# Optimization experiments

Measured on AMD Instinct MI355X. Metric: run time of the kernel, lower is better.

## Reference

```python
import jax, jax.numpy as jnp
import numpy as np

N = 50000      # nodes
E = 800000     # edges (before self loops)
D_IN = 128
HID = 64
HEADS = 8
D_OUT = 10


def setup_inputs() -> dict:
    key = jax.random.key(0)
    ks = jax.random.split(key, 16)
    sc = 0.05
    x = jax.random.normal(ks[0], (N, D_IN), dtype=jnp.float32)
    edge_index = jax.random.randint(ks[1], (2, E), 0, N, dtype=jnp.int64)
    return {
        "x": x,
        "edge_index": edge_index,
        "W1": jax.random.normal(ks[2], (HEADS * HID, D_IN), dtype=jnp.float32) * sc,
        "a1_src": jax.random.normal(ks[3], (HEADS, HID), dtype=jnp.float32) * sc,
        "a1_dst": jax.random.normal(ks[4], (HEADS, HID), dtype=jnp.float32) * sc,
        "b1": jnp.zeros((HEADS * HID,), jnp.float32),
        "W2": jax.random.normal(ks[5], (HID, HEADS * HID), dtype=jnp.float32) * sc,
        "a2_src": jax.random.normal(ks[6], (1, HID), dtype=jnp.float32) * sc,
        "a2_dst": jax.random.normal(ks[7], (1, HID), dtype=jnp.float32) * sc,
        "b2": jnp.zeros((HID,), jnp.float32),
        "W3": jax.random.normal(ks[8], (HID, HID), dtype=jnp.float32) * sc,
        "a3_src": jax.random.normal(ks[9], (1, HID), dtype=jnp.float32) * sc,
        "a3_dst": jax.random.normal(ks[10], (1, HID), dtype=jnp.float32) * sc,
        "b3": jnp.zeros((HID,), jnp.float32),
        "Wc": jax.random.normal(ks[11], (D_OUT, HID), dtype=jnp.float32) * sc,
        "bc": jnp.zeros((D_OUT,), jnp.float32),
    }


def gat_conv(x, src, dst, W, a_src, a_dst, b, concat):
    """PyG GATConv (eval mode, add_self_loops already applied to src/dst)."""
    heads, out_ch = a_src.shape
    n = x.shape[0]
    h = (x @ W.T).reshape(n, heads, out_ch)          # [N, H, C]
    a_s = jnp.einsum('nhc,hc->nh', h, a_src)          # [N, H]
    a_d = jnp.einsum('nhc,hc->nh', h, a_dst)          # [N, H]
    e = jax.nn.leaky_relu(a_s[src] + a_d[dst], 0.2)   # [Etot, H]
    # segment softmax over incoming edges of each destination node
    m = jax.ops.segment_max(e, dst, num_segments=n)
    ex = jnp.exp(e - m[dst])
    s = jax.ops.segment_sum(ex, dst, num_segments=n)
    alpha = ex / (s[dst] + 1e-16)                     # [Etot, H]
    out = jax.ops.segment_sum(h[src] * alpha[:, :, None], dst, num_segments=n)
    if concat:
        out = out.reshape(n, heads * out_ch)
    else:
        out = out.mean(axis=1)
    return out + b


def reference(x, edge_index, W1, a1_src, a1_dst, b1, W2, a2_src, a2_dst, b2,
              W3, a3_src, a3_dst, b3, Wc, bc):
    loops = jnp.arange(N, dtype=edge_index.dtype)
    src = jnp.concatenate([edge_index[0], loops])
    dst = jnp.concatenate([edge_index[1], loops])
    h = jax.nn.elu(gat_conv(x, src, dst, W1, a1_src, a1_dst, b1, True))
    h = jax.nn.elu(gat_conv(h, src, dst, W2, a2_src, a2_dst, b2, False))
    h = jax.nn.elu(gat_conv(h, src, dst, W3, a3_src, a3_dst, b3, False))
    return h @ Wc.T + bc
```

## Files before the change

### kernel.cpp

```cpp
#include <hip/hip_runtime.h>
#include <math.h>

#define N_NODES 50000
#define N_EDGES 800000
#define ETOT    (N_EDGES + N_NODES)

typedef short bf16x8 __attribute__((ext_vector_type(8)));
typedef float f32x4  __attribute__((ext_vector_type(4)));
typedef float f32x2  __attribute__((ext_vector_type(2)));

__device__ __forceinline__ float b2f(unsigned int u16) {
    return __uint_as_float(u16 << 16);
}
__device__ __forceinline__ unsigned short f2b(float f) {
    unsigned int u = __float_as_uint(f);
    u += 0x7fffu + ((u >> 16) & 1u);
    return (unsigned short)(u >> 16);
}

__global__ __launch_bounds__(256) void k_prep(const float* __restrict__ x,
                                              const float* __restrict__ w1,
                                              const float* __restrict__ w2,
                                              const float* __restrict__ w3,
                                              unsigned short* __restrict__ xb,
                                              unsigned short* __restrict__ o1,
                                              unsigned short* __restrict__ o2,
                                              unsigned short* __restrict__ o3,
                                              int* __restrict__ deg,
                                              int* __restrict__ flag) {
    int i = blockIdx.x * 256 + threadIdx.x;
    if (i < N_NODES) deg[i] = 0;
    if (i == 0) *flag = 0;
    if (i < 512 * 128 / 4) {
        float4 v = ((const float4*)w1)[i];
        ushort2* o = (ushort2*)(o1 + i * 4);
        o[0] = make_ushort2(f2b(v.x), f2b(v.y));
        o[1] = make_ushort2(f2b(v.z), f2b(v.w));
    }
    if (i < 64 * 512 / 4) {
        float4 v = ((const float4*)w2)[i];
        ushort2* o = (ushort2*)(o2 + i * 4);
        o[0] = make_ushort2(f2b(v.x), f2b(v.y));
        o[1] = make_ushort2(f2b(v.z), f2b(v.w));
    }
    if (i < 64 * 64 / 4) {
        float4 v = ((const float4*)w3)[i];
        ushort2* o = (ushort2*)(o3 + i * 4);
        o[0] = make_ushort2(f2b(v.x), f2b(v.y));
        o[1] = make_ushort2(f2b(v.z), f2b(v.w));
    }
    if (i < N_NODES * 128 / 8) {
        const float4* xp = (const float4*)x + (size_t)i * 2;
        float4 v0 = xp[0], v1 = xp[1];
        unsigned int u0 = (unsigned int)f2b(v0.x) | ((unsigned int)f2b(v0.y) << 16);
        unsigned int u1 = (unsigned int)f2b(v0.z) | ((unsigned int)f2b(v0.w) << 16);
        unsigned int u2 = (unsigned int)f2b(v1.x) | ((unsigned int)f2b(v1.y) << 16);
        unsigned int u3 = (unsigned int)f2b(v1.z) | ((unsigned int)f2b(v1.w) << 16);
        *(uint4*)(xb + (size_t)i * 8) = make_uint4(u0, u1, u2, u3);
    }
}

__global__ void k_detect(const int* __restrict__ idx, int* __restrict__ flag) {
    int i = blockIdx.x * blockDim.x + threadIdx.x;
    int v = idx[2 * i + 1];
    unsigned long long any = __ballot(v != 0);
    if ((threadIdx.x & 63) == 0 && any) atomicOr(flag, 1);
}

__device__ __forceinline__ int edge_src(const int* idx, int e, int is32) {
    return is32 ? idx[e] : idx[2 * e];
}
__device__ __forceinline__ int edge_dst(const int* idx, int e, int is32) {
    return is32 ? idx[N_EDGES + e] : idx[2 * (N_EDGES + e)];
}

__global__ void k_degree(const int* __restrict__ idx, const int* __restrict__ flag,
                         int* __restrict__ deg) {
    int e = blockIdx.x * blockDim.x + threadIdx.x;
    if (e >= ETOT) return;
    int is32 = *flag;
    int d = (e < N_EDGES) ? edge_dst(idx, e, is32) : (e - N_EDGES);
    atomicAdd(&deg[d], 1);
}

__global__ __launch_bounds__(256) void k_scan1(const int* __restrict__ deg,
                                               int* __restrict__ rowptr,
                                               int* __restrict__ bsum) {
    __shared__ int sd[256];
    int t = threadIdx.x;
    int i = blockIdx.x * 256 + t;
    int v = (i < N_NODES) ? deg[i] : 0;
    sd[t] = v;
    __syncthreads();
#pragma unroll
    for (int off = 1; off < 256; off <<= 1) {
        int a = (t >= off) ? sd[t - off] : 0;
        __syncthreads();
        sd[t] += a;
        __syncthreads();
    }
    if (i < N_NODES) rowptr[i] = sd[t] - v;
    if (t == 255) bsum[blockIdx.x] = sd[255];
}

__global__ __launch_bounds__(256) void k_scan2(int* __restrict__ bsum,
                                               int* __restrict__ boff,
                                               int* __restrict__ rowptr,
                                               int nb) {
    __shared__ int sd[256];
    int t = threadIdx.x;
    int v = (t < nb) ? bsum[t] : 0;
    sd[t] = v;
    __syncthreads();
#pragma unroll
    for (int off = 1; off < 256; off <<= 1) {
        int a = (t >= off) ? sd[t - off] : 0;
        __syncthreads();
        sd[t] += a;
        __syncthreads();
    }
    boff[t] = sd[t] - v;
    if (t == 255) rowptr[N_NODES] = sd[255];
}

__global__ __launch_bounds__(256) void k_scan3(int* __restrict__ rowptr,
                                               const int* __restrict__ boff,
                                               int* __restrict__ cursor) {
    int i = blockIdx.x * 256 + threadIdx.x;
    if (i >= N_NODES) return;
    int r = rowptr[i] + boff[blockIdx.x];
    rowptr[i] = r;
    cursor[i] = r;
}

__global__ void k_scatter(const int* __restrict__ idx, const int* __restrict__ flag,
                          int* __restrict__ cursor, int* __restrict__ col) {
    int e = blockIdx.x * blockDim.x + threadIdx.x;
    if (e >= ETOT) return;
    int is32 = *flag;
    int s, d;
    if (e < N_EDGES) { s = edge_src(idx, e, is32); d = edge_dst(idx, e, is32); }
    else             { s = d = e - N_EDGES; }
    int pos = atomicAdd(&cursor[d], 1);
    col[pos] = s;
}

template<int AFP32>
__global__ __launch_bounds__(256) void k_gemm(const float* __restrict__ Af,
                                              const unsigned short* __restrict__ Ab,
                                              const unsigned short* __restrict__ W,
                                              unsigned short* __restrict__ C,
                                              const float* __restrict__ a_src,
                                              const float* __restrict__ a_dst,
                                              float* __restrict__ asb,
                                              float* __restrict__ adb,
                                              int M, int K, int Nout, int Hstr) {
    __shared__ unsigned short As[64 * 40];
    __shared__ unsigned short Bs[64 * 40];
    __shared__ float red_s[4][64];
    __shared__ float red_d[4][64];
    int t = threadIdx.x;
    int w = t >> 6, l = t & 63;
    int quad = l >> 4, lm = l & 15;
    int m0 = blockIdx.y * 64, n0 = blockIdx.x * 64;
    int hd = blockIdx.x;
    int lr = t >> 2;
    int lc = (t & 3) * 8;

    f32x4 acc[4];
#pragma unroll
    for (int r = 0; r < 4; ++r) acc[r] = (f32x4){0.f, 0.f, 0.f, 0.f};

    for (int k0 = 0; k0 < K; k0 += 32) {
        int m = m0 + lr;
        if (AFP32) {
            float4 a0 = {0.f,0.f,0.f,0.f}, a1 = {0.f,0.f,0.f,0.f};
            if (m < M) {
                const float4* ap = (const float4*)(Af + (size_t)m * K + k0 + lc);
                a0 = ap[0]; a1 = ap[1];
            }
            unsigned int u0 = (unsigned int)f2b(a0.x) | ((unsigned int)f2b(a0.y) << 16);
            unsigned int u1 = (unsigned int)f2b(a0.z) | ((unsigned int)f2b(a0.w) << 16);
            unsigned int u2 = (unsigned int)f2b(a1.x) | ((unsigned int)f2b(a1.y) << 16);
            unsigned int u3 = (unsigned int)f2b(a1.z) | ((unsigned int)f2b(a1.w) << 16);
            *(uint4*)&As[lr * 40 + lc] = make_uint4(u0, u1, u2, u3);
        } else {
            uint4 av = make_uint4(0, 0, 0, 0);
            if (m < M) av = *(const uint4*)(Ab + (size_t)m * K + k0 + lc);
            *(uint4*)&As[lr * 40 + lc] = av;
        }
        uint4 bv = *(const uint4*)(W + (size_t)(n0 + lr) * K + k0 + lc);
        *(uint4*)&Bs[lr * 40 + lc] = bv;
        __syncthreads();

        bf16x8 bfrag = *(const bf16x8*)&Bs[(w * 16 + lm) * 40 + quad * 8];
#pragma unroll
        for (int r = 0; r < 4; ++r) {
            bf16x8 afrag = *(const bf16x8*)&As[(r * 16 + lm) * 40 + quad * 8];
            acc[r] = __builtin_amdgcn_mfma_f32_16x16x32_bf16(afrag, bfrag, acc[r], 0, 0, 0);
        }
        __syncthreads();
    }

#pragma unroll
    for (int r = 0; r < 4; ++r)
#pragma unroll
        for (int g = 0; g < 4; ++g) {
            int m = m0 + r * 16 + quad * 4 + g;
            if (m < M) C[(size_t)m * Nout + n0 + w * 16 + lm] = f2b(acc[r][g]);
        }

    float as = a_src[hd * 64 + w * 16 + lm];
    float ad = a_dst[hd * 64 + w * 16 + lm];
#pragma unroll
    for (int r = 0; r < 4; ++r) {
#pragma unroll
        for (int g = 0; g < 4; ++g) {
            float vs = acc[r][g] * as;
            float vd = acc[r][g] * ad;
#pragma unroll
            for (int off = 1; off < 16; off <<= 1) {
                vs += __shfl_xor(vs, off);
                vd += __shfl_xor(vd, off);
            }
            if (lm == 0) {
                red_s[w][r * 16 + quad * 4 + g] = vs;
                red_d[w][r * 16 + quad * 4 + g] = vd;
            }
        }
    }
    __syncthreads();
    if (t < 64) {
        float vs = red_s[0][t] + red_s[1][t] + red_s[2][t] + red_s[3][t];
        float vd = red_d[0][t] + red_d[1][t] + red_d[2][t] + red_d[3][t];
        int m = m0 + t;
        if (m < M) {
            asb[(size_t)m * Hstr + hd] = vs;
            adb[(size_t)m * Hstr + hd] = vd;
        }
    }
}

__device__ __forceinline__ void agg8_acc(float t, float adn, uint4 hv,
                                         float& ssum, f32x2* o2) {
    float e = t + adn;
    e = fmaxf(e, 0.2f * e);
    float ex = __expf(e);
    ssum += ex;
    f32x2 ex2 = {ex, ex};
    f32x2 f;
    f.x = __uint_as_float(hv.x << 16); f.y = __uint_as_float(hv.x & 0xffff0000u);
    asm("v_pk_fma_f32 %0, %1, %2, %0" : "+v"(o2[0]) : "v"(f), "v"(ex2));
    f.x = __uint_as_float(hv.y << 16); f.y = __uint_as_float(hv.y & 0xffff0000u);
    asm("v_pk_fma_f32 %0, %1, %2, %0" : "+v"(o2[1]) : "v"(f), "v"(ex2));
    f.x = __uint_as_float(hv.z << 16); f.y = __uint_as_float(hv.z & 0xffff0000u);
    asm("v_pk_fma_f32 %0, %1, %2, %0" : "+v"(o2[2]) : "v"(f), "v"(ex2));
    f.x = __uint_as_float(hv.w << 16); f.y = __uint_as_float(hv.w & 0xffff0000u);
    asm("v_pk_fma_f32 %0, %1, %2, %0" : "+v"(o2[3]) : "v"(f), "v"(ex2));
}

__global__ __launch_bounds__(256) void k_agg8(const unsigned short* __restrict__ h,
                                              const float* __restrict__ asrc,
                                              const float* __restrict__ adst,
                                              const int* __restrict__ rowptr,
                                              const int* __restrict__ col,
                                              const float* __restrict__ bias,
                                              unsigned short* __restrict__ out) {
    int n = blockIdx.x * 4 + (threadIdx.x >> 6);
    if (n >= N_NODES) return;
    int l = threadIdx.x & 63;
    int j = l >> 3;
    int lbase = l << 3;
    int start = rowptr[n], end = rowptr[n + 1];
    float adn = adst[(n << 3) + j];

    float ssum = 0.f;
    f32x2 o2[4];
#pragma unroll
    for (int i = 0; i < 4; ++i) o2[i] = (f32x2){0.f, 0.f};

    int k = start;
    int kA = (start + 3) & ~3;
    if (kA > end) kA = end;
    for (; k < kA; ++k) {
        int s = col[k];
        float t = asrc[((unsigned)s << 3) + (unsigned)j];
        uint4 hv = *(const uint4*)(h + ((unsigned)s << 9) + (unsigned)lbase);
        agg8_acc(t, adn, hv, ssum, o2);
    }
    int kEnd4 = kA + ((end - kA) & ~3);
    if (k < kEnd4) {
        int4 cN = *(const int4*)(col + k);
        for (; k < kEnd4; k += 4) {
            int4 c = cN;
            if (k + 8 <= kEnd4) cN = *(const int4*)(col + k + 4);
            float t0 = asrc[((unsigned)c.x << 3) + (unsigned)j];
            float t1 = asrc[((unsigned)c.y << 3) + (unsigned)j];
            float t2 = asrc[((unsigned)c.z << 3) + (unsigned)j];
            float t3 = asrc[((unsigned)c.w << 3) + (unsigned)j];
            uint4 hv0 = *(const uint4*)(h + ((unsigned)c.x << 9) + (unsigned)lbase);
            uint4 hv1 = *(const uint4*)(h + ((unsigned)c.y << 9) + (unsigned)lbase);
            uint4 hv2 = *(const uint4*)(h + ((unsigned)c.z << 9) + (unsigned)lbase);
            uint4 hv3 = *(const uint4*)(h + ((unsigned)c.w << 9) + (unsigned)lbase);
            agg8_acc(t0, adn, hv0, ssum, o2);
            agg8_acc(t1, adn, hv1, ssum, o2);
            agg8_acc(t2, adn, hv2, ssum, o2);
            agg8_acc(t3, adn, hv3, ssum, o2);
        }
    }
    for (; k < end; ++k) {
        int s = col[k];
        float t = asrc[((unsigned)s << 3) + (unsigned)j];
        uint4 hv = *(const uint4*)(h + ((unsigned)s << 9) + (unsigned)lbase);
        agg8_acc(t, adn, hv, ssum, o2);
    }

    float inv = 1.f / (ssum + 1e-16f);
    unsigned int p[4];
#pragma unroll
    for (int i = 0; i < 4; ++i) {
        float v0 = o2[i].x * inv + bias[lbase + 2 * i];
        float v1 = o2[i].y * inv + bias[lbase + 2 * i + 1];
        v0 = (v0 > 0.f) ? v0 : expm1f(v0);
        v1 = (v1 > 0.f) ? v1 : expm1f(v1);
        p[i] = (unsigned int)f2b(v0) | ((unsigned int)f2b(v1) << 16);
    }
    *(uint4*)(out + (size_t)n * 512 + lbase) = make_uint4(p[0], p[1], p[2], p[3]);
}

__global__ __launch_bounds__(256) void k_agg1(const unsigned short* __restrict__ h,
                                              const float* __restrict__ asrc,
                                              const float* __restrict__ adst,
                                              const int* __restrict__ rowptr,
                                              const int* __restrict__ col,
                                              const float* __restrict__ bias,
                                              unsigned short* __restrict__ out) {
    int n = blockIdx.x * 4 + (threadIdx.x >> 6);
    if (n >= N_NODES) return;
    int l = threadIdx.x & 63;
    int start = rowptr[n], end = rowptr[n + 1];
    float adn = adst[n];

    float ssum = 0.f, o = 0.f;
    int k = start;
    int kA = (start + 3) & ~3;
    if (kA > end) kA = end;
    for (; k < kA; ++k) {
        int s = col[k];
        float t = asrc[s];
        float hf = b2f(h[((unsigned)s << 6) + (unsigned)l]);
        float e = t + adn; e = fmaxf(e, 0.2f * e);
        float ex = __expf(e);
        ssum += ex; o += ex * hf;
    }
    int kEnd4 = kA + ((end - kA) & ~3);
    if (k < kEnd4) {
        int4 cN = *(const int4*)(col + k);
        for (; k < kEnd4; k += 4) {
            int4 c = cN;
            if (k + 8 <= kEnd4) cN = *(const int4*)(col + k + 4);
            float t0 = asrc[c.x], t1 = asrc[c.y], t2 = asrc[c.z], t3 = asrc[c.w];
            unsigned short q0 = h[((unsigned)c.x << 6) + (unsigned)l];
            unsigned short q1 = h[((unsigned)c.y << 6) + (unsigned)l];
            unsigned short q2 = h[((unsigned)c.z << 6) + (unsigned)l];
            unsigned short q3 = h[((unsigned)c.w << 6) + (unsigned)l];
            float e0 = t0 + adn; e0 = fmaxf(e0, 0.2f * e0);
            float ex0 = __expf(e0); ssum += ex0; o += ex0 * b2f(q0);
            float e1 = t1 + adn; e1 = fmaxf(e1, 0.2f * e1);
            float ex1 = __expf(e1); ssum += ex1; o += ex1 * b2f(q1);
            float e2 = t2 + adn; e2 = fmaxf(e2, 0.2f * e2);
            float ex2 = __expf(e2); ssum += ex2; o += ex2 * b2f(q2);
            float e3 = t3 + adn; e3 = fmaxf(e3, 0.2f * e3);
            float ex3 = __expf(e3); ssum += ex3; o += ex3 * b2f(q3);
        }
    }
    for (; k < end; ++k) {
        int s = col[k];
        float t = asrc[s];
        float hf = b2f(h[((unsigned)s << 6) + (unsigned)l]);
        float e = t + adn; e = fmaxf(e, 0.2f * e);
        float ex = __expf(e);
        ssum += ex; o += ex * hf;
    }
    float v = o / (ssum + 1e-16f) + bias[l];
    v = (v > 0.f) ? v : expm1f(v);
    out[(size_t)n * 64 + l] = f2b(v);
}

__global__ __launch_bounds__(256) void k_classifier(const unsigned short* __restrict__ h,
                                                    const float* __restrict__ Wc,
                                                    const float* __restrict__ bc,
                                                    float* __restrict__ out) {
    __shared__ float sW[640];
    for (int i = threadIdx.x; i < 640; i += blockDim.x) sW[i] = Wc[i];
    __syncthreads();
    int idx = blockIdx.x * blockDim.x + threadIdx.x;
    if (idx >= N_NODES * 10) return;
    int n = idx / 10, d = idx - n * 10;
    const unsigned short* hr = h + (size_t)n * 64;
    const float* wr = sW + d * 64;
    float acc = 0.f;
#pragma unroll
    for (int c = 0; c < 64; ++c) acc += b2f(hr[c]) * wr[c];
    out[idx] = acc + bc[d];
}

extern "C" void kernel_launch(void* const* d_in, const int* in_sizes, int n_in,
                              void* d_out, int out_size, void* d_ws, size_t ws_size,
                              hipStream_t stream) {
    const float* x    = (const float*)d_in[0];
    const int*   eidx = (const int*)  d_in[1];
    const float* W1   = (const float*)d_in[2];
    const float* a1s  = (const float*)d_in[3];
    const float* a1d  = (const float*)d_in[4];
    const float* b1   = (const float*)d_in[5];
    const float* W2   = (const float*)d_in[6];
    const float* a2s  = (const float*)d_in[7];
    const float* a2d  = (const float*)d_in[8];
    const float* b2   = (const float*)d_in[9];
    const float* W3   = (const float*)d_in[10];
    const float* a3s  = (const float*)d_in[11];
    const float* a3d  = (const float*)d_in[12];
    const float* b3   = (const float*)d_in[13];
    const float* Wc   = (const float*)d_in[14];
    const float* bc   = (const float*)d_in[15];
    float* out = (float*)d_out;

    float* asbuf = (float*)d_ws;
    float* adbuf = asbuf + (size_t)N_NODES * 8;
    unsigned short* h1  = (unsigned short*)(adbuf + (size_t)N_NODES * 8);
    unsigned short* x2  = h1  + (size_t)N_NODES * 512;
    unsigned short* h2  = x2  + (size_t)N_NODES * 512;
    unsigned short* x3  = h2  + (size_t)N_NODES * 64;
    unsigned short* h3  = x3  + (size_t)N_NODES * 64;
    unsigned short* x4  = h3  + (size_t)N_NODES * 64;
    unsigned short* xb  = x4  + (size_t)N_NODES * 64;
    unsigned short* W1b = xb  + (size_t)N_NODES * 128;
    unsigned short* W2b = W1b + 512 * 128;
    unsigned short* W3b = W2b + 64 * 512;
    int* ibase  = (int*)(W3b + 64 * 64);
    int* deg    = ibase;
    int* flag   = deg + N_NODES;
    int* rowptr = flag + 1;
    int* cursor = rowptr + N_NODES + 1;
    int* bsum   = cursor + N_NODES;
    int* boff   = bsum + 256;
    int* col    = boff + 256;

    dim3 blk(256);
    const int SCAN_BLOCKS = (N_NODES + 255) / 256;
    const int PREP_BLOCKS = (N_NODES * 128 / 8 + 255) / 256;

    k_prep<<<PREP_BLOCKS, blk, 0, stream>>>(x, W1, W2, W3, xb, W1b, W2b, W3b, deg, flag);
    k_detect<<<32, blk, 0, stream>>>(eidx, flag);
    k_degree<<<(ETOT + 255) / 256, blk, 0, stream>>>(eidx, flag, deg);
    k_scan1<<<SCAN_BLOCKS, blk, 0, stream>>>(deg, rowptr, bsum);
    k_scan2<<<1, blk, 0, stream>>>(bsum, boff, rowptr, SCAN_BLOCKS);
    k_scan3<<<SCAN_BLOCKS, blk, 0, stream>>>(rowptr, boff, cursor);
    k_scatter<<<(ETOT + 255) / 256, blk, 0, stream>>>(eidx, flag, cursor, col);

    int mblocks = (N_NODES + 63) / 64;
    int nblocks = N_NODES / 4;

    k_gemm<0><<<dim3(8, mblocks), blk, 0, stream>>>((const float*)0, xb, W1b, h1,
                                                    a1s, a1d, asbuf, adbuf,
                                                    N_NODES, 128, 512, 8);
    k_agg8<<<nblocks, blk, 0, stream>>>(h1, asbuf, adbuf, rowptr, col, b1, x2);

    k_gemm<0><<<dim3(1, mblocks), blk, 0, stream>>>((const float*)0, x2, W2b, h2,
                                                    a2s, a2d, asbuf, adbuf,
                                                    N_NODES, 512, 64, 1);
    k_agg1<<<nblocks, blk, 0, stream>>>(h2, asbuf, adbuf, rowptr, col, b2, x3);

    k_gemm<0><<<dim3(1, mblocks), blk, 0, stream>>>((const float*)0, x3, W3b, h3,
                                                    a3s, a3d, asbuf, adbuf,
                                                    N_NODES, 64, 64, 1);
    k_agg1<<<nblocks, blk, 0, stream>>>(h3, asbuf, adbuf, rowptr, col, b3, x4);

    k_classifier<<<(N_NODES * 10 + 255) / 256, blk, 0, stream>>>(x4, Wc, bc, out);
}
```

Baseline: 512.7 us.

## Pad CSR rows to multiples of four and double-buffer aggregation gathers

The scan now rounds each node's degree up to a multiple of four and fills the padding slots with node 0, so every CSR row starts 16-byte aligned and can be read with int4 loads without scalar prologue or epilogue loops. The aggregation kernels keep the real degree separate, mask padded slots to zero weight, and use an A/B double buffer so the gathers for the next four neighbours are issued before the current four are accumulated. This targets gather latency and loop overhead in the memory-bound aggregation. In exchange the col array grows and the kernels do wasted loads for padding slots. COL_CAP is defined but not visibly used, so whether the workspace allocation grew to hold the padding cannot be checked from the visible code.

```diff
diff --git a/kernel.cpp b/kernel.cpp
--- a/kernel.cpp
+++ b/kernel.cpp
@@ -4,6 +4,7 @@
 #define N_NODES 50000
 #define N_EDGES 800000
 #define ETOT    (N_EDGES + N_NODES)
+#define COL_CAP (ETOT + 3 * N_NODES + 16)
 
 typedef short bf16x8 __attribute__((ext_vector_type(8)));
 typedef float f32x4  __attribute__((ext_vector_type(4)));
@@ -89,7 +90,7 @@
     __shared__ int sd[256];
     int t = threadIdx.x;
     int i = blockIdx.x * 256 + t;
-    int v = (i < N_NODES) ? deg[i] : 0;
+    int v = (i < N_NODES) ? ((deg[i] + 3) & ~3) : 0;
     sd[t] = v;
     __syncthreads();
 #pragma unroll
@@ -125,12 +126,21 @@
 
 __global__ __launch_bounds__(256) void k_scan3(int* __restrict__ rowptr,
                                                const int* __restrict__ boff,
-                                               int* __restrict__ cursor) {
+                                               const int* __restrict__ deg,
+                                               int* __restrict__ cursor,
+                                               int* __restrict__ col) {
     int i = blockIdx.x * 256 + threadIdx.x;
+    if (i == 0) {
+        int tot = rowptr[N_NODES];
+        for (int q = 0; q < 16; ++q) col[tot + q] = 0;
+    }
     if (i >= N_NODES) return;
     int r = rowptr[i] + boff[blockIdx.x];
     rowptr[i] = r;
     cursor[i] = r;
+    int d = deg[i];
+    int pd = (d + 3) & ~3;
+    for (int p = r + d; p < r + pd; ++p) col[p] = 0;
 }
 
 __global__ void k_scatter(const int* __restrict__ idx, const int* __restrict__ flag,
@@ -241,28 +251,11 @@
     }
 }
 
-__device__ __forceinline__ void agg8_acc(float t, float adn, uint4 hv,
-                                         float& ssum, f32x2* o2) {
-    float e = t + adn;
-    e = fmaxf(e, 0.2f * e);
-    float ex = __expf(e);
-    ssum += ex;
-    f32x2 ex2 = {ex, ex};
-    f32x2 f;
-    f.x = __uint_as_float(hv.x << 16); f.y = __uint_as_float(hv.x & 0xffff0000u);
-    asm("v_pk_fma_f32 %0, %1, %2, %0" : "+v"(o2[0]) : "v"(f), "v"(ex2));
-    f.x = __uint_as_float(hv.y << 16); f.y = __uint_as_float(hv.y & 0xffff0000u);
-    asm("v_pk_fma_f32 %0, %1, %2, %0" : "+v"(o2[1]) : "v"(f), "v"(ex2));
-    f.x = __uint_as_float(hv.z << 16); f.y = __uint_as_float(hv.z & 0xffff0000u);
-    asm("v_pk_fma_f32 %0, %1, %2, %0" : "+v"(o2[2]) : "v"(f), "v"(ex2));
-    f.x = __uint_as_float(hv.w << 16); f.y = __uint_as_float(hv.w & 0xffff0000u);
-    asm("v_pk_fma_f32 %0, %1, %2, %0" : "+v"(o2[3]) : "v"(f), "v"(ex2));
-}
-
 __global__ __launch_bounds__(256) void k_agg8(const unsigned short* __restrict__ h,
                                               const float* __restrict__ asrc,
                                               const float* __restrict__ adst,
                                               const int* __restrict__ rowptr,
+                                              const int* __restrict__ degv,
                                               const int* __restrict__ col,
                                               const float* __restrict__ bias,
                                               unsigned short* __restrict__ out) {
@@ -270,50 +263,89 @@
     if (n >= N_NODES) return;
     int l = threadIdx.x & 63;
     int j = l >> 3;
-    int lbase = l << 3;
-    int start = rowptr[n], end = rowptr[n + 1];
-    float adn = adst[(n << 3) + j];
+    unsigned lbase = (unsigned)(l << 3);
+    int start = rowptr[n];
+    int end   = start + degv[n];
+    float adn = adst[((unsigned)n << 3) + (unsigned)j];
 
     float ssum = 0.f;
     f32x2 o2[4];
 #pragma unroll
     for (int i = 0; i < 4; ++i) o2[i] = (f32x2){0.f, 0.f};
 
+    float tA0, tA1, tA2, tA3, tB0, tB1, tB2, tB3;
+    uint4 hA0, hA1, hA2, hA3, hB0, hB1, hB2, hB3;
+    int4 cA, cB;
+
+#define GATH8(c, T0, T1, T2, T3, H0, H1, H2, H3)                              \
+    T0 = asrc[(((unsigned)(c).x) << 3) + (unsigned)j];                        \
+    T1 = asrc[(((unsigned)(c).y) << 3) + (unsigned)j];                        \
+    T2 = asrc[(((unsigned)(c).z) << 3) + (unsigned)j];                        \
+    T3 = asrc[(((unsigned)(c).w) << 3) + (unsigned)j];                        \
+    H0 = *(const uint4*)(h + (((unsigned)(c).x) << 9) + lbase);               \
+    H1 = *(const uint4*)(h + (((unsigned)(c).y) << 9) + lbase);               \
+    H2 = *(const uint4*)(h + (((unsigned)(c).z) << 9) + lbase);               \
+    H3 = *(const uint4*)(h + (((unsigned)(c).w) << 9) + lbase);
+
+#define ASLOT8(IDX, TT, HH, rem)                                              \
+    {                                                                         \
+        float e = TT + adn;                                                   \
+        e = fmaxf(e, 0.2f * e);                                               \
+        float ex = __expf(e);                                                 \
+        ex = ((IDX) < (rem)) ? ex : 0.f;                                      \
+        ssum += ex;                                                           \
+        f32x2 ex2 = {ex, ex};                                                 \
+        f32x2 f;                                                              \
+        f.x = __uint_as_float((HH).x << 16);                                  \
+        f.y = __uint_as_float((HH).x & 0xffff0000u);                          \
+        asm("v_pk_fma_f32 %0, %1, %2, %0" : "+v"(o2[0]) : "v"(f), "v"(ex2));  \
+        f.x = __uint_as_float((HH).y << 16);                                  \
+        f.y = __uint_as_float((HH).y & 0xffff0000u);                          \
+        asm("v_pk_fma_f32 %0, %1, %2, %0" : "+v"(o2[1]) : "v"(f), "v"(ex2));  \
+        f.x = __uint_as_float((HH).z << 16);                                  \
+        f.y = __uint_as_float((HH).z & 0xffff0000u);                          \
+        asm("v_pk_fma_f32 %0, %1, %2, %0" : "+v"(o2[2]) : "v"(f), "v"(ex2));  \
+        f.x = __uint_as_float((HH).w << 16);                                  \
+        f.y = __uint_as_float((HH).w & 0xffff0000u);                          \
+        asm("v_pk_fma_f32 %0, %1, %2, %0" : "+v"(o2[3]) : "v"(f), "v"(ex2));  \
+    }
+
     int k = start;
-    int kA = (start + 3) & ~3;
-    if (kA > end) kA = end;
-    for (; k < kA; ++k) {
-        int s = col[k];
-        float t = asrc[((unsigned)s << 3) + (unsigned)j];
-        uint4 hv = *(const uint4*)(h + ((unsigned)s << 9) + (unsigned)lbase);
-        agg8_acc(t, adn, hv, ssum, o2);
-    }
-    int kEnd4 = kA + ((end - kA) & ~3);
-    if (k < kEnd4) {
-        int4 cN = *(const int4*)(col + k);
-        for (; k < kEnd4; k += 4) {
-            int4 c = cN;
-            if (k + 8 <= kEnd4) cN = *(const int4*)(col + k + 4);
-            float t0 = asrc[((unsigned)c.x << 3) + (unsigned)j];
-            float t1 = asrc[((unsigned)c.y << 3) + (unsigned)j];
-            float t2 = asrc[((unsigned)c.z << 3) + (unsigned)j];
-            float t3 = asrc[((unsigned)c.w << 3) + (unsigned)j];
-            uint4 hv0 = *(const uint4*)(h + ((unsigned)c.x << 9) + (unsigned)lbase);
-            uint4 hv1 = *(const uint4*)(h + ((unsigned)c.y << 9) + (unsigned)lbase);
-            uint4 hv2 = *(const uint4*)(h + ((unsigned)c.z << 9) + (unsigned)lbase);
-            uint4 hv3 = *(const uint4*)(h + ((unsigned)c.w << 9) + (unsigned)lbase);
-            agg8_acc(t0, adn, hv0, ssum, o2);
-            agg8_acc(t1, adn, hv1, ssum, o2);
-            agg8_acc(t2, adn, hv2, ssum, o2);
-            agg8_acc(t3, adn, hv3, ssum, o2);
-        }
-    }
-    for (; k < end; ++k) {
-        int s = col[k];
-        float t = asrc[((unsigned)s << 3) + (unsigned)j];
-        uint4 hv = *(const uint4*)(h + ((unsigned)s << 9) + (unsigned)lbase);
-        agg8_acc(t, adn, hv, ssum, o2);
-    }
+    cA = *(const int4*)(col + k);
+    cB = *(const int4*)(col + k + 4);
+    GATH8(cA, tA0, tA1, tA2, tA3, hA0, hA1, hA2, hA3);
+    for (;;) {
+        bool hasB = (k + 4 < end);
+        if (hasB) {
+            GATH8(cB, tB0, tB1, tB2, tB3, hB0, hB1, hB2, hB3);
+            cA = *(const int4*)(col + k + 8);
+        }
+        {
+            int rem = end - k;
+            ASLOT8(0, tA0, hA0, rem);
+            ASLOT8(1, tA1, hA1, rem);
+            ASLOT8(2, tA2, hA2, rem);
+            ASLOT8(3, tA3, hA3, rem);
+        }
+        k += 4;
+        if (!hasB) break;
+        bool hasA = (k + 4 < end);
+        if (hasA) {
+            GATH8(cA, tA0, tA1, tA2, tA3, hA0, hA1, hA2, hA3);
+            cB = *(const int4*)(col + k + 8);
+        }
+        {
+            int rem = end - k;
+            ASLOT8(0, tB0, hB0, rem);
+            ASLOT8(1, tB1, hB1, rem);
+            ASLOT8(2, tB2, hB2, rem);
+            ASLOT8(3, tB3, hB3, rem);
+        }
+        k += 4;
+        if (!hasA) break;
+    }
+#undef GATH8
+#undef ASLOT8
 
     float inv = 1.f / (ssum + 1e-16f);
     unsigned int p[4];
@@ -332,56 +364,79 @@
                                               const float* __restrict__ asrc,
                                               const float* __restrict__ adst,
                                               const int* __restrict__ rowptr,
+                                              const int* __restrict__ degv,
                                               const int* __restrict__ col,
                                               const float* __restrict__ bias,
                                               unsigned short* __restrict__ out) {
     int n = blockIdx.x * 4 + (threadIdx.x >> 6);
     if (n >= N_NODES) return;
     int l = threadIdx.x & 63;
-    int start = rowptr[n], end = rowptr[n + 1];
+    int start = rowptr[n];
+    int end   = start + degv[n];
     float adn = adst[n];
 
     float ssum = 0.f, o = 0.f;
+    float tA0, tA1, tA2, tA3, tB0, tB1, tB2, tB3;
+    unsigned short qA0, qA1, qA2, qA3, qB0, qB1, qB2, qB3;
+    int4 cA, cB;
+
+#define GATH1(c, T0, T1, T2, T3, Q0, Q1, Q2, Q3)                              \
+    T0 = asrc[(unsigned)(c).x];                                               \
+    T1 = asrc[(unsigned)(c).y];                                               \
+    T2 = asrc[(unsigned)(c).z];                                               \
+    T3 = asrc[(unsigned)(c).w];                                               \
+    Q0 = h[(((unsigned)(c).x) << 6) + (unsigned)l];                           \
+    Q1 = h[(((unsigned)(c).y) << 6) + (unsigned)l];                           \
+    Q2 = h[(((unsigned)(c).z) << 6) + (unsigned)l];                           \
+    Q3 = h[(((unsigned)(c).w) << 6) + (unsigned)l];
+
+#define ASLOT1(IDX, TT, QQ, rem)                                              \
+    {                                                                         \
+        float e = TT + adn;                                                   \
+        e = fmaxf(e, 0.2f * e);                                               \
+        float ex = __expf(e);                                                 \
+        ex = ((IDX) < (rem)) ? ex : 0.f;                                      \
+        ssum += ex;                                                           \
+        o += ex * b2f(QQ);                                                    \
+    }
+
     int k = start;
-    int kA = (start + 3) & ~3;
-    if (kA > end) kA = end;
-    for (; k < kA; ++k) {
-        int s = col[k];
-        float t = asrc[s];
-        float hf = b2f(h[((unsigned)s << 6) + (unsigned)l]);
-        float e = t + adn; e = fmaxf(e, 0.2f * e);
-        float ex = __expf(e);
-        ssum += ex; o += ex * hf;
-    }
-    int kEnd4 = kA + ((end - kA) & ~3);
-    if (k < kEnd4) {
-        int4 cN = *(const int4*)(col + k);
-        for (; k < kEnd4; k += 4) {
-            int4 c = cN;
-            if (k + 8 <= kEnd4) cN = *(const int4*)(col + k + 4);
-            float t0 = asrc[c.x], t1 = asrc[c.y], t2 = asrc[c.z], t3 = asrc[c.w];
-            unsigned short q0 = h[((unsigned)c.x << 6) + (unsigned)l];
-            unsigned short q1 = h[((unsigned)c.y << 6) + (unsigned)l];
-            unsigned short q2 = h[((unsigned)c.z << 6) + (unsigned)l];
-            unsigned short q3 = h[((unsigned)c.w << 6) + (unsigned)l];
-            float e0 = t0 + adn; e0 = fmaxf(e0, 0.2f * e0);
-            float ex0 = __expf(e0); ssum += ex0; o += ex0 * b2f(q0);
-            float e1 = t1 + adn; e1 = fmaxf(e1, 0.2f * e1);
-            float ex1 = __expf(e1); ssum += ex1; o += ex1 * b2f(q1);
-            float e2 = t2 + adn; e2 = fmaxf(e2, 0.2f * e2);
-            float ex2 = __expf(e2); ssum += ex2; o += ex2 * b2f(q2);
-            float e3 = t3 + adn; e3 = fmaxf(e3, 0.2f * e3);
-            float ex3 = __expf(e3); ssum += ex3; o += ex3 * b2f(q3);
-        }
-    }
-    for (; k < end; ++k) {
-        int s = col[k];
-        float t = asrc[s];
-        float hf = b2f(h[((unsigned)s << 6) + (unsigned)l]);
-        float e = t + adn; e = fmaxf(e, 0.2f * e);
-        float ex = __expf(e);
-        ssum += ex; o += ex * hf;
-    }
+    cA = *(const int4*)(col + k);
+    cB = *(const int4*)(col + k + 4);
+    GATH1(cA, tA0, tA1, tA2, tA3, qA0, qA1, qA2, qA3);
+    for (;;) {
+        bool hasB = (k + 4 < end);
+        if (hasB) {
+            GATH1(cB, tB0, tB1, tB2, tB3, qB0, qB1, qB2, qB3);
+            cA = *(const int4*)(col + k + 8);
+        }
+        {
+            int rem = end - k;
+            ASLOT1(0, tA0, qA0, rem);
+            ASLOT1(1, tA1, qA1, rem);
+            ASLOT1(2, tA2, qA2, rem);
+            ASLOT1(3, tA3, qA3, rem);
+        }
+        k += 4;
+        if (!hasB) break;
+        bool hasA = (k + 4 < end);
+        if (hasA) {
+            GATH1(cA, tA0, tA1, tA2, tA3, qA0, qA1, qA2, qA3);
+            cB = *(const int4*)(col + k + 8);
+        }
+        {
+            int rem = end - k;
+            ASLOT1(0, tB0, qB0, rem);
+            ASLOT1(1, tB1, qB1, rem);
+            ASLOT1(2, tB2, qB2, rem);
+            ASLOT1(3, tB3, qB3, rem);
+        }
+        k += 4;
+        if (!hasA) break;
+    }
+#undef GATH1
+#undef ASLOT1
+
     float v = o / (ssum + 1e-16f) + bias[l];
     v = (v > 0.f) ? v : expm1f(v);
     out[(size_t)n * 64 + l] = f2b(v);
@@ -456,7 +511,7 @@
     k_degree<<<(ETOT + 255) / 256, blk, 0, stream>>>(eidx, flag, deg);
     k_scan1<<<SCAN_BLOCKS, blk, 0, stream>>>(deg, rowptr, bsum);
     k_scan2<<<1, blk, 0, stream>>>(bsum, boff, rowptr, SCAN_BLOCKS);
-    k_scan3<<<SCAN_BLOCKS, blk, 0, stream>>>(rowptr, boff, cursor);
+    k_scan3<<<SCAN_BLOCKS, blk, 0, stream>>>(rowptr, boff, deg, cursor, col);
     k_scatter<<<(ETOT + 255) / 256, blk, 0, stream>>>(eidx, flag, cursor, col);
 
     int mblocks = (N_NODES + 63) / 64;
@@ -465,17 +520,17 @@
     k_gemm<0><<<dim3(8, mblocks), blk, 0, stream>>>((const float*)0, xb, W1b, h1,
                                                     a1s, a1d, asbuf, adbuf,
                                                     N_NODES, 128, 512, 8);
-    k_agg8<<<nblocks, blk, 0, stream>>>(h1, asbuf, adbuf, rowptr, col, b1, x2);
+    k_agg8<<<nblocks, blk, 0, stream>>>(h1, asbuf, adbuf, rowptr, deg, col, b1, x2);
 
     k_gemm<0><<<dim3(1, mblocks), blk, 0, stream>>>((const float*)0, x2, W2b, h2,
                                                     a2s, a2d, asbuf, adbuf,
                                                     N_NODES, 512, 64, 1);
-    k_agg1<<<nblocks, blk, 0, stream>>>(h2, asbuf, adbuf, rowptr, col, b2, x3);
+    k_agg1<<<nblocks, blk, 0, stream>>>(h2, asbuf, adbuf, rowptr, deg, col, b2, x3);
 
     k_gemm<0><<<dim3(1, mblocks), blk, 0, stream>>>((const float*)0, x3, W3b, h3,
                                                     a3s, a3d, asbuf, adbuf,
                                                     N_NODES, 64, 64, 1);
-    k_agg1<<<nblocks, blk, 0, stream>>>(h3, asbuf, adbuf, rowptr, col, b3, x4);
+    k_agg1<<<nblocks, blk, 0, stream>>>(h3, asbuf, adbuf, rowptr, deg, col, b3, x4);
 
     k_classifier<<<(N_NODES * 10 + 255) / 256, blk, 0, stream>>>(x4, Wc, bc, out);
 }
```

After: 503.2 us. No clear change (-1.9%).
